# Kernel tuning notes

Hardware: AMD Instinct MI355X
Metric: run time of the kernel (lower is better)

## Reference

```python
import jax, jax.numpy as jnp
import numpy as np

EPS = 1e-3  # keras LayerNormalization default epsilon

def _ln(x, gamma, beta):
    m = jnp.mean(x, axis=-1, keepdims=True)
    v = jnp.var(x, axis=-1, keepdims=True)
    return gamma * (x - m) * jax.lax.rsqrt(v + EPS) + beta

def setup_inputs() -> dict:
    B, T, F, H = 256, 128, 4, 512  # T*F must equal H (skip-connection constraint in context GRN)
    D = T * F
    key = jax.random.key(0)
    ks = jax.random.split(key, 16)
    s = lambda fan: 1.0 / np.sqrt(fan)
    inp = {
        "inputs": jax.random.normal(ks[0], (B, T, F), jnp.float32),
        # context GRN (input dim D = T*F = H)
        "W1c": jax.random.normal(ks[1], (D, H), jnp.float32) * s(D),
        "b1c": jnp.zeros((H,), jnp.float32),
        "W2c": jax.random.normal(ks[2], (H, H), jnp.float32) * s(H),
        "b2c": jnp.zeros((H,), jnp.float32),
        "Wgc": jax.random.normal(ks[3], (H, H), jnp.float32) * s(H),
        "bgc": jnp.zeros((H,), jnp.float32),
        "gamma_c": jnp.ones((H,), jnp.float32),
        "beta_c": jnp.zeros((H,), jnp.float32),
        # softmax variable-selection head
        "Wsel": jax.random.normal(ks[4], (H, F), jnp.float32) * s(H),
        "bsel": jnp.zeros((F,), jnp.float32),
        # F per-variable GRNs, batched over leading F axis (input dim 1)
        "w1": jax.random.normal(ks[5], (F, H), jnp.float32),
        "b1": jnp.zeros((F, H), jnp.float32),
        "W2": jax.random.normal(ks[6], (F, H, H), jnp.float32) * s(H),
        "b2": jnp.zeros((F, H), jnp.float32),
        "Wg": jax.random.normal(ks[7], (F, H, H), jnp.float32) * s(H),
        "bg": jnp.zeros((F, H), jnp.float32),
        "gamma": jnp.ones((F, H), jnp.float32),
        "beta": jnp.zeros((F, H), jnp.float32),
    }
    return inp

def reference(inputs, W1c, b1c, W2c, b2c, Wgc, bgc, gamma_c, beta_c,
              Wsel, bsel, w1, b1, W2, b2, Wg, bg, gamma, beta):
    B, T, F = inputs.shape
    # ---- context GRN on flattened inputs (skip == flat since T*F == H) ----
    flat = inputs.reshape(B, T * F)
    x = jax.nn.elu(flat @ W1c + b1c)
    x = x @ W2c + b2c
    g = jax.nn.sigmoid(x @ Wgc + bgc)
    ctx = _ln(g * x + (1.0 - g) * flat, gamma_c, beta_c)
    # ---- softmax selection weights over variables ----
    sel = jax.nn.softmax(ctx @ Wsel + bsel)  # [B, F]
    # ---- per-variable GRNs, batched over F (input is scalar per variable) ----
    v = inputs[..., None]                              # [B,T,F,1] (skip path)
    x1 = jax.nn.elu(v * w1 + b1)                       # [B,T,F,H]
    x2 = jnp.einsum('btfh,fhk->btfk', x1, W2) + b2     # dense2
    gv = jax.nn.sigmoid(jnp.einsum('btfh,fhk->btfk', x2, Wg) + bg)
    gated = gv * x2 + (1.0 - gv) * v                   # skip broadcasts [B,T,F,1]
    tv = _ln(gated, gamma, beta)                       # [B,T,F,H]
    # ---- weighted sum over variables ----
    selected = jnp.einsum('btfh,bf->bth', tv, sel)     # [B,T,H]
    sel_weights = jnp.tile(sel[:, None, None, :], (1, T, 1, 1))  # [B,T,1,F]
    return selected, sel_weights
```

## Files before the change

### kernel.cpp

```cpp
#include <hip/hip_runtime.h>
#include <math.h>


#define H 512
#define NF 4
#define MTOT 32768

typedef unsigned short u16;
typedef unsigned int u32;
typedef __attribute__((ext_vector_type(8))) short short8;
typedef __attribute__((ext_vector_type(4))) float f32x4;
typedef __attribute__((ext_vector_type(4))) u32 u32x4;

__device__ __forceinline__ u16 f2bf(float x) {
  union { float f; u32 u; } v; v.f = x;
  return (u16)((v.u + 0x7fffu + ((v.u >> 16) & 1u)) >> 16);
}
__device__ __forceinline__ float bf2f(u32 h16) {
  union { u32 u; float f; } v; v.u = h16 << 16;
  return v.f;
}
__device__ __forceinline__ float elu_f(float x) {
  return x > 0.0f ? x : (__expf(x) - 1.0f);
}
__device__ __forceinline__ float sigmoid_f(float x) {
  return __builtin_amdgcn_rcpf(1.0f + __expf(-x));
}
__device__ __forceinline__ u32 cvtpk(float lo, float hi) {
  u32 r;
  asm("v_cvt_pk_bf16_f32 %0, %1, %2" : "=v"(r) : "v"(lo), "v"(hi));
  return r;
}
template <int CTRL>
__device__ __forceinline__ float dppadd(float v) {
  int t = __builtin_amdgcn_update_dpp(0, __float_as_int(v), CTRL, 0xF, 0xF, true);
  return v + __int_as_float(t);
}
__device__ __forceinline__ float red16(float v) {
  v = dppadd<0xB1>(v);
  v = dppadd<0x4E>(v);
  v = dppadd<0x141>(v);
  v = dppadd<0x140>(v);
  return v;
}

__device__ __forceinline__ void glld16(const void* g, void* l) {
  __builtin_amdgcn_global_load_lds(
      (const __attribute__((address_space(1))) u32*)(unsigned long long)(uintptr_t)g,
      (__attribute__((address_space(3))) u32*)(u32)(uintptr_t)l, 16, 0, 0);
}

#define MFMA16(a, b, c) __builtin_amdgcn_mfma_f32_16x16x32_bf16((a), (b), (c), 0, 0, 0)

__device__ __forceinline__ int sA_idx(int m, int n) {
  return m * 512 + ((((n >> 3) ^ (m & 7)) << 3) + (n & 7));
}

__device__ __forceinline__ void gridbar(u32* cnt, u32 target) {
  __syncthreads();
  __threadfence();
  if (threadIdx.x == 0) {
    __hip_atomic_fetch_add(cnt, 1u, __ATOMIC_RELEASE, __HIP_MEMORY_SCOPE_AGENT);
    while (__hip_atomic_load(cnt, __ATOMIC_ACQUIRE, __HIP_MEMORY_SCOPE_AGENT) < target)
      __builtin_amdgcn_s_sleep(8);
  }
  __syncthreads();
  __threadfence();
}

struct TileCtx {
  int tid, wid, lane, quad, col;
};

__global__ __launch_bounds__(256)
void pack_all(const float* __restrict__ W2, const float* __restrict__ Wg,
              const float* __restrict__ W1c, const float* __restrict__ W2c,
              const float* __restrict__ Wgc,
              u16* __restrict__ W2p, u16* __restrict__ Wgp, u16* __restrict__ Cp,
              u32* __restrict__ bar) {
  int g = blockIdx.x * 256 + threadIdx.x;
  if (g == 0) { bar[0] = 0; bar[1] = 0; }
  int r = g & 32767; int mat = g >> 15;
  if (mat >= 11) return;
  const float* src; u16* dst;
  if (mat < 4)      { src = W2 + (size_t)mat * 262144;       dst = W2p + (size_t)mat * 262144; }
  else if (mat < 8) { src = Wg + (size_t)(mat - 4) * 262144; dst = Wgp + (size_t)(mat - 4) * 262144; }
  else              { src = (mat == 8 ? W1c : (mat == 9 ? W2c : Wgc));
                      dst = Cp + (size_t)(mat - 8) * 262144; }
  dst += (size_t)r * 8;
  int lane = r & 63;
  int n, k0;
  if (mat == 8 || mat == 9) {
    int nb = r >> 12, kk = (r >> 8) & 15, ntg = (r >> 6) & 3;
    n  = nb * 64 + ntg * 16 + (lane & 15);
    k0 = kk * 32 + (lane >> 4) * 8;
  } else {
    int nt = (r >> 6) & 31, kk = (r >> 11) & 15;
    n  = nt * 16 + (lane & 15);
    k0 = kk * 32 + (lane >> 4) * 8;
  }
  short8 pk;
  #pragma unroll
  for (int j = 0; j < 8; ++j) pk[j] = (short)f2bf(src[(size_t)(k0 + j) * H + n]);
  *(short8*)dst = pk;
}

__device__ __forceinline__ void slab_kloop(const TileCtx& c, const u16* Wslab,
                                           u16* sA, u16* sB0, u16* sB1,
                                           f32x4 acc[4]) {
  #pragma unroll 1
  for (int kk = 0; kk < 16; ++kk) {
    if (kk < 15)
      glld16(Wslab + (kk + 1) * 2048 + c.tid * 8,
             (((kk + 1) & 1) ? sB1 : sB0) + c.tid * 8);
    const u16* bp = ((kk & 1) ? sB1 : sB0) + c.wid * 512 + c.lane * 8;
    short8 bb = *(const short8*)(bp);
    const int kq = kk * 4 + c.quad;
    const int s0 = (kq ^ (c.col & 7)) * 8;
    short8 a0 = *(const short8*)&sA[(     c.col) * 512 + s0];
    short8 a1 = *(const short8*)&sA[(16 + c.col) * 512 + s0];
    short8 a2 = *(const short8*)&sA[(32 + c.col) * 512 + s0];
    short8 a3 = *(const short8*)&sA[(48 + c.col) * 512 + s0];
    acc[0] = MFMA16(a0, bb, acc[0]);
    acc[1] = MFMA16(a1, bb, acc[1]);
    acc[2] = MFMA16(a2, bb, acc[2]);
    acc[3] = MFMA16(a3, bb, acc[3]);
    __syncthreads();
  }
}

__global__ __launch_bounds__(256)
void ctx_fused(const float* __restrict__ in, const u16* __restrict__ Cp,
               const float* __restrict__ b1c, const float* __restrict__ b2c,
               const float* __restrict__ bgc,
               const float* __restrict__ gamma_c, const float* __restrict__ beta_c,
               const float* __restrict__ Wsel, const float* __restrict__ bsel,
               u16* __restrict__ x1g, u16* __restrict__ xg,
               float* __restrict__ sel_ws, float* __restrict__ selw_out,
               u32* __restrict__ bar)
{
  __shared__ __align__(16) u16 smem[49152];
  TileCtx c;
  c.tid = threadIdx.x; c.wid = c.tid >> 6; c.lane = c.tid & 63;
  c.quad = c.lane >> 4; c.col = c.lane & 15;
  const int blk = blockIdx.x;
  const int mb = blk >> 3, nb = blk & 7;
  const int m0 = mb * 64;

  {
    u16* const sA  = smem;
    u16* const sB0 = smem + 32768;
    u16* const sB1 = smem + 34816;
    const u16* Wslab = Cp + (size_t)nb * 32768;
    glld16(Wslab + c.tid * 8, sB0 + c.tid * 8);
    {
      const int m = c.tid >> 2;
      const int kb = (c.tid & 3) * 128;
      const float* rowp = in + (size_t)(m0 + m) * H;
      #pragma unroll
      for (int gg = 0; gg < 16; ++gg) {
        const int ge = (gg + (c.tid & 3) * 4) & 15;
        const int k = kb + ge * 8;
        float4 v0 = *(const float4*)&rowp[k];
        float4 v1 = *(const float4*)&rowp[k + 4];
        u32x4 pk4;
        pk4.x = cvtpk(v0.x, v0.y); pk4.y = cvtpk(v0.z, v0.w);
        pk4.z = cvtpk(v1.x, v1.y); pk4.w = cvtpk(v1.z, v1.w);
        const int grp = (k >> 3) ^ (m & 7);
        *(u32x4*)&sA[m * 512 + grp * 8] = pk4;
      }
    }
    __syncthreads();
    f32x4 acc[4];
    #pragma unroll
    for (int mt = 0; mt < 4; ++mt) acc[mt] = (f32x4){0,0,0,0};
    slab_kloop(c, Wslab, sA, sB0, sB1, acc);
    const int n = nb * 64 + c.wid * 16 + c.col;
    const float bv = b1c[n];
    #pragma unroll
    for (int mt = 0; mt < 4; ++mt)
      #pragma unroll
      for (int reg = 0; reg < 4; ++reg) {
        const int m = m0 + mt * 16 + c.quad * 4 + reg;
        x1g[(size_t)m * H + n] = f2bf(elu_f(acc[mt][reg] + bv));
      }
  }
  gridbar(bar + 0, 32);

  {
    u16* const sA  = smem;
    u16* const sB0 = smem + 32768;
    u16* const sB1 = smem + 34816;
    const u16* Wslab = Cp + 262144 + (size_t)nb * 32768;
    glld16(Wslab + c.tid * 8, sB0 + c.tid * 8);
    {
      const int m = c.tid >> 2;
      const int kb = (c.tid & 3) * 128;
      const u16* rowp = x1g + (size_t)(m0 + m) * H;
      #pragma unroll
      for (int gg = 0; gg < 16; ++gg) {
        const int ge = (gg + (c.tid & 3) * 4) & 15;
        const int k = kb + ge * 8;
        short8 w = *(const short8*)&rowp[k];
        const int grp = (k >> 3) ^ (m & 7);
        *(short8*)&sA[m * 512 + grp * 8] = w;
      }
    }
    __syncthreads();
    f32x4 acc[4];
    #pragma unroll
    for (int mt = 0; mt < 4; ++mt) acc[mt] = (f32x4){0,0,0,0};
    slab_kloop(c, Wslab, sA, sB0, sB1, acc);
    const int n = nb * 64 + c.wid * 16 + c.col;
    const float bv = b2c[n];
    #pragma unroll
    for (int mt = 0; mt < 4; ++mt)
      #pragma unroll
      for (int reg = 0; reg < 4; ++reg) {
        const int m = m0 + mt * 16 + c.quad * 4 + reg;
        xg[(size_t)m * H + n] = f2bf(acc[mt][reg] + bv);
      }
  }
  gridbar(bar + 1, 32);
  if (blk >= 16) return;

  {
    u16* const sA  = smem;
    u16* const sB0 = smem + 8192;
    u16* const sB1 = smem + 24576;
    float* const sRedF = (float*)sB0;
    float* const sZp  = sRedF + 1024;
    float* const sZf  = sRedF + 1792;
    float* const sSel = sRedF + 1952;
    const int b0 = blk * 16;
    const u16* Wgcp = Cp + 524288;

    #pragma unroll
    for (int i = 0; i < 8; ++i)
      glld16(Wgcp + (i * 256 + c.tid) * 8, sB0 + (i * 256 + c.tid) * 8);

    {
      const int m  = c.tid >> 4;
      const int kb = (c.tid & 15) * 32;
      const u16* rowp = xg + (size_t)(b0 + m) * H;
      #pragma unroll
      for (int gg = 0; gg < 4; ++gg) {
        const int ge = (gg + (c.tid & 15)) & 3;
        const int k = kb + ge * 8;
        short8 w = *(const short8*)&rowp[k];
        const int grp = (k >> 3) ^ (m & 7);
        *(short8*)&sA[m * 512 + grp * 8] = w;
      }
    }
    __syncthreads();

    f32x4 acc8[8];
    #pragma unroll
    for (int j = 0; j < 8; ++j) acc8[j] = (f32x4){0,0,0,0};

    #pragma unroll 1
    for (int kk = 0; kk < 16; ++kk) {
      if (kk < 15) {
        const u16* src = Wgcp + (kk + 1) * 16384;
        u16* dst = ((kk + 1) & 1) ? sB1 : sB0;
        #pragma unroll
        for (int i = 0; i < 8; ++i)
          glld16(src + (i * 256 + c.tid) * 8, dst + (i * 256 + c.tid) * 8);
      }
      const u16* bp = (kk & 1) ? sB1 : sB0;
      short8 bb[8];
      #pragma unroll
      for (int j = 0; j < 8; ++j)
        bb[j] = *(const short8*)(bp + ((c.wid * 8 + j) * 64 + c.lane) * 8);
      const int kq = kk * 4 + c.quad;
      const int s0 = (kq ^ (c.col & 7)) * 8;
      short8 a0 = *(const short8*)&sA[c.col * 512 + s0];
      #pragma unroll
      for (int j = 0; j < 8; ++j) acc8[j] = MFMA16(a0, bb[j], acc8[j]);
      __syncthreads();
    }

    {
      float bv[8];
      #pragma unroll
      for (int j = 0; j < 8; ++j) bv[j] = bgc[c.wid * 128 + j * 16 + c.col];
      #pragma unroll
      for (int j = 0; j < 8; ++j) {
        const int n = c.wid * 128 + j * 16 + c.col;
        #pragma unroll
        for (int reg = 0; reg < 4; ++reg) {
          const int m = c.quad * 4 + reg;
          const float xv = bf2f(sA[sA_idx(m, n)]);
          const float fl = in[(size_t)(b0 + m) * H + n];
          const float gv = sigmoid_f(acc8[j][reg] + bv[j]);
          acc8[j][reg] = gv * xv + (1.0f - gv) * fl;
        }
      }
    }

    {
      float rs[4], rq[4];
      #pragma unroll
      for (int reg = 0; reg < 4; ++reg) {
        rs[reg] = 0.f; rq[reg] = 0.f;
        #pragma unroll
        for (int j = 0; j < 8; ++j) {
          const float gt = acc8[j][reg];
          rs[reg] += gt; rq[reg] += gt * gt;
        }
        rs[reg] = red16(rs[reg]);
        rq[reg] = red16(rq[reg]);
      }
      if (c.col == 0) {
        #pragma unroll
        for (int reg = 0; reg < 4; ++reg) {
          const int m = c.quad * 4 + reg;
          float2 sq; sq.x = rs[reg]; sq.y = rq[reg];
          *(float2*)&sRedF[m * 20 + c.wid * 2] = sq;
        }
      }
    }
    __syncthreads();
    if (c.tid < 16) {
      const int row = c.tid;
      float s = 0.f, q = 0.f;
      #pragma unroll
      for (int jj = 0; jj < 2; ++jj) {
        float4 v = *(float4*)&sRedF[row * 20 + jj * 4];
        s += v.x + v.z; q += v.y + v.w;
      }
      const float mu = s * (1.0f / H);
      const float rstd = rsqrtf(q * (1.0f / H) - mu * mu + 1e-3f);
      float2 mr; mr.x = mu; mr.y = rstd;
      *(float2*)&sRedF[640 + row * 2] = mr;
    }
    __syncthreads();

    {
      float gm[8], bt[8]; float4 ws4[8];
      #pragma unroll
      for (int j = 0; j < 8; ++j) {
        const int n = c.wid * 128 + j * 16 + c.col;
        gm[j] = gamma_c[n]; bt[j] = beta_c[n];
        ws4[j] = *(const float4*)&Wsel[n * NF];
      }
      #pragma unroll
      for (int reg = 0; reg < 4; ++reg) {
        const int m = c.quad * 4 + reg;
        float2 mr = *(float2*)&sRedF[640 + m * 2];
        float zp[4] = {0.f, 0.f, 0.f, 0.f};
        #pragma unroll
        for (int j = 0; j < 8; ++j) {
          const float ctxv = gm[j] * ((acc8[j][reg] - mr.x) * mr.y) + bt[j];
          zp[0] = fmaf(ctxv, ws4[j].x, zp[0]);
          zp[1] = fmaf(ctxv, ws4[j].y, zp[1]);
          zp[2] = fmaf(ctxv, ws4[j].z, zp[2]);
          zp[3] = fmaf(ctxv, ws4[j].w, zp[3]);
        }
        #pragma unroll
        for (int f = 0; f < 4; ++f) zp[f] = red16(zp[f]);
        if (c.col == 0) {
          #pragma unroll
          for (int f = 0; f < 4; ++f) sZp[(m * 4 + c.wid) * 4 + f] = zp[f];
        }
      }
    }
    __syncthreads();
    if (c.tid < 64) {
      const int m = c.tid >> 2, f = c.tid & 3;
      float z = bsel[f];
      #pragma unroll
      for (int w = 0; w < 4; ++w) z += sZp[(m * 4 + w) * 4 + f];
      sZf[m * 4 + f] = z;
    }
    __syncthreads();
    if (c.tid < 16) {
      const int m = c.tid;
      float z0 = sZf[m*4], z1 = sZf[m*4+1], z2 = sZf[m*4+2], z3 = sZf[m*4+3];
      float mx = fmaxf(fmaxf(z0, z1), fmaxf(z2, z3));
      float e0 = __expf(z0-mx), e1 = __expf(z1-mx), e2 = __expf(z2-mx), e3 = __expf(z3-mx);
      float inv = __builtin_amdgcn_rcpf(e0 + e1 + e2 + e3);
      sSel[m*4]   = e0*inv; sSel[m*4+1] = e1*inv;
      sSel[m*4+2] = e2*inv; sSel[m*4+3] = e3*inv;
      sel_ws[(b0+m)*NF]   = e0*inv; sel_ws[(b0+m)*NF+1] = e1*inv;
      sel_ws[(b0+m)*NF+2] = e2*inv; sel_ws[(b0+m)*NF+3] = e3*inv;
    }
    __syncthreads();
    {
      const int m = c.tid >> 4;
      const int jb = (c.tid & 15) * 32;
      float4 v; v.x = sSel[m*4]; v.y = sSel[m*4+1]; v.z = sSel[m*4+2]; v.w = sSel[m*4+3];
      #pragma unroll
      for (int j = 0; j < 8; ++j)
        *(float4*)&selw_out[(size_t)(b0 + m) * H + jb + j * 4] = v;
    }
  }
}


__device__ __forceinline__ void stage_slice(int wid, int lane, const u16* chunk, u16* dstbuf) {
  const u16* src = chunk + wid * 2048 + lane * 8;
  u16* dst = dstbuf + lane * 8;
  glld16(src,        dst);
  glld16(src + 512,  dst + 512);
  glld16(src + 1024, dst + 1024);
  glld16(src + 1536, dst + 1536);
}

__device__ __forceinline__ void gemm_kloop_nb(const TileCtx& c, const u16* Wp,
                                              const u16* sA, u16* sBw,
                                              f32x4 acc[4][4]) {
  #pragma unroll 1
  for (int kk = 0; kk < 16; ++kk) {
    if (kk < 15) {
      stage_slice(c.wid, c.lane, Wp + (kk + 1) * 16384, sBw + ((kk + 1) & 1) * 2048);
      asm volatile("s_waitcnt vmcnt(4)" ::: "memory");
    } else {
      asm volatile("s_waitcnt vmcnt(0)" ::: "memory");
    }
    __builtin_amdgcn_sched_barrier(0);
    const u16* bp = sBw + (kk & 1) * 2048 + c.lane * 8;
    short8 bb[4];
    #pragma unroll
    for (int nt = 0; nt < 4; ++nt) bb[nt] = *(const short8*)(bp + nt * 512);
    const int kq = kk * 4 + c.quad;
    const int s0 = (kq ^ (c.col & 7)) * 8;
    __builtin_amdgcn_s_setprio(1);
    #pragma unroll
    for (int mt = 0; mt < 4; ++mt) {
      short8 a = *(const short8*)&sA[(mt * 16 + c.col) * 512 + s0];
      #pragma unroll
      for (int nt = 0; nt < 4; ++nt)
        acc[mt][nt] = MFMA16(a, bb[nt], acc[mt][nt]);
    }
    __builtin_amdgcn_s_setprio(0);
  }
}

__device__ __forceinline__ void store_x2_pair_n(const TileCtx& c, u16* sA,
                                                int mt, int n, u32 o01, u32 o23) {
  const bool even = (c.lane & 1) == 0;
  const u32 send = even ? o23 : o01;
  const u32 recv = (u32)__builtin_amdgcn_update_dpp(0, (int)send, 0xB1, 0xF, 0xF, true);
  const u32 hi = even ? recv : o23;
  const u32 lo = even ? o01 : recv;
  const u32 dlo = __builtin_amdgcn_perm(hi, lo, 0x05040100u);
  const u32 dhi = __builtin_amdgcn_perm(hi, lo, 0x07060302u);
  const int np = n & ~1;
  const int mA = mt * 16 + c.quad * 4 + (even ? 0 : 2);
  const int iA = mA * 512 + ((((np >> 3) ^ (mA & 7)) << 3) + (np & 7));
  const int mB = mA + 1;
  const int iB = mB * 512 + ((((np >> 3) ^ (mB & 7)) << 3) + (np & 7));
  *(u32*)&sA[iA] = dlo;
  *(u32*)&sA[iB] = dhi;
}

__device__ __forceinline__ void ln_reduce8(const TileCtx& c, float* sRedF,
                                           f32x4 acc[4][4]) {
  #pragma unroll
  for (int mt = 0; mt < 4; ++mt) {
    float rs[4], rq[4];
    #pragma unroll
    for (int reg = 0; reg < 4; ++reg) {
      rs[reg] = 0.f; rq[reg] = 0.f;
      #pragma unroll
      for (int nt = 0; nt < 4; ++nt) {
        const float gt = acc[mt][nt][reg];
        rs[reg] += gt; rq[reg] += gt * gt;
      }
      rs[reg] = red16(rs[reg]);
      rq[reg] = red16(rq[reg]);
    }
    if (c.col == 0) {
      #pragma unroll
      for (int reg = 0; reg < 4; ++reg) {
        const int m = mt * 16 + c.quad * 4 + reg;
        float2 sq; sq.x = rs[reg]; sq.y = rq[reg];
        *(float2*)&sRedF[m * 20 + c.wid * 2] = sq;
      }
    }
  }
  __syncthreads();
  if (c.tid < 64) {
    const int row = c.tid;
    float s = 0.f, q = 0.f;
    #pragma unroll
    for (int jj = 0; jj < 4; ++jj) {
      float4 v = *(float4*)&sRedF[row * 20 + jj * 4];
      s += v.x + v.z; q += v.y + v.w;
    }
    const float mu = s * (1.0f / H);
    const float rstd = rsqrtf(q * (1.0f / H) - mu * mu + 1e-3f);
    float2 mr; mr.x = mu; mr.y = rstd;
    *(float2*)&sRedF[1280 + row * 2] = mr;
  }
  __syncthreads();
}

__global__ __launch_bounds__(512, 2)
void vsn_mfma(const float* __restrict__ in,
              const float* __restrict__ w1, const float* __restrict__ b1,
              const float* __restrict__ b2, const float* __restrict__ bg,
              const float* __restrict__ gamma, const float* __restrict__ beta,
              const u16* __restrict__ W2p, const u16* __restrict__ Wgp,
              const float* __restrict__ sel_ws,
              float* __restrict__ out)
{
  __shared__ __align__(16) u16 smem[65536];
  u16* const sA  = smem;
  u16* const sB  = smem + 32768;
  float* const sRedF = (float*)smem;

  TileCtx c;
  c.tid = threadIdx.x; c.wid = c.tid >> 6; c.lane = c.tid & 63;
  c.quad = c.lane >> 4; c.col = c.lane & 15;
  u16* const sBw = sB + c.wid * 4096;
  const int row0 = blockIdx.x * 64;
  const int bidx = row0 >> 7;

  f32x4 outacc[4][4];
  #pragma unroll
  for (int mt = 0; mt < 4; ++mt)
    #pragma unroll
    for (int nt = 0; nt < 4; ++nt) outacc[mt][nt] = (f32x4){0,0,0,0};

  stage_slice(c.wid, c.lane, W2p, sBw);

  #pragma unroll 1
  for (int f = 0; f < NF; ++f) {
    const u16* W2f = W2p + (size_t)f * 262144;
    const u16* Wgf = Wgp + (size_t)f * 262144;

    {
      const int m  = c.tid >> 3;
      const int kb = (c.tid & 7) * 64;
      const float v = in[(size_t)(row0 + m) * NF + f];
      const float* w1f = w1 + f * H;
      const float* b1f = b1 + f * H;
      #pragma unroll
      for (int gg = 0; gg < 8; ++gg) {
        const int ge = (gg + (c.tid & 7)) & 7;
        const int k = kb + ge * 8;
        float4 wv0 = *(const float4*)&w1f[k];
        float4 wv1 = *(const float4*)&w1f[k + 4];
        float4 bv0 = *(const float4*)&b1f[k];
        float4 bv1 = *(const float4*)&b1f[k + 4];
        u32x4 pk4;
        pk4.x = cvtpk(elu_f(fmaf(v, wv0.x, bv0.x)), elu_f(fmaf(v, wv0.y, bv0.y)));
        pk4.y = cvtpk(elu_f(fmaf(v, wv0.z, bv0.z)), elu_f(fmaf(v, wv0.w, bv0.w)));
        pk4.z = cvtpk(elu_f(fmaf(v, wv1.x, bv1.x)), elu_f(fmaf(v, wv1.y, bv1.y)));
        pk4.w = cvtpk(elu_f(fmaf(v, wv1.z, bv1.z)), elu_f(fmaf(v, wv1.w, bv1.w)));
        const int grp = (k >> 3) ^ (m & 7);
        *(u32x4*)&sA[m * 512 + grp * 8] = pk4;
      }
    }
    __syncthreads();

    f32x4 acc[4][4];
    #pragma unroll
    for (int mt = 0; mt < 4; ++mt)
      #pragma unroll
      for (int nt = 0; nt < 4; ++nt) acc[mt][nt] = (f32x4){0,0,0,0};

    gemm_kloop_nb(c, W2f, sA, sBw, acc);
    __syncthreads();

    stage_slice(c.wid, c.lane, Wgf, sBw);

    u32 x2p[4][4][2];
    {
      float bv[4];
      #pragma unroll
      for (int nt = 0; nt < 4; ++nt) bv[nt] = b2[f * H + c.wid * 64 + nt * 16 + c.col];
      #pragma unroll
      for (int mt = 0; mt < 4; ++mt)
        #pragma unroll
        for (int nt = 0; nt < 4; ++nt) {
          const u32 o01 = cvtpk(acc[mt][nt][0] + bv[nt], acc[mt][nt][1] + bv[nt]);
          const u32 o23 = cvtpk(acc[mt][nt][2] + bv[nt], acc[mt][nt][3] + bv[nt]);
          x2p[mt][nt][0] = o01; x2p[mt][nt][1] = o23;
          store_x2_pair_n(c, sA, mt, c.wid * 64 + nt * 16 + c.col, o01, o23);
        }
    }
    __syncthreads();

    #pragma unroll
    for (int mt = 0; mt < 4; ++mt)
      #pragma unroll
      for (int nt = 0; nt < 4; ++nt) acc[mt][nt] = (f32x4){0,0,0,0};
    gemm_kloop_nb(c, Wgf, sA, sBw, acc);

    {
      const float selw = sel_ws[bidx * NF + f];
      float bv[4];
      #pragma unroll
      for (int nt = 0; nt < 4; ++nt) bv[nt] = bg[f * H + c.wid * 64 + nt * 16 + c.col];
      #pragma unroll
      for (int mt = 0; mt < 4; ++mt) {
        float vr[4];
        #pragma unroll
        for (int reg = 0; reg < 4; ++reg)
          vr[reg] = in[(size_t)(row0 + mt * 16 + c.quad * 4 + reg) * NF + f];
        #pragma unroll
        for (int nt = 0; nt < 4; ++nt)
          #pragma unroll
          for (int reg = 0; reg < 4; ++reg) {
            const u32 w = x2p[mt][nt][reg >> 1];
            const float x2v = bf2f((reg & 1) ? (w >> 16) : (w & 0xffffu));
            const float gv = sigmoid_f(acc[mt][nt][reg] + bv[nt]);
            acc[mt][nt][reg] = gv * x2v + (1.0f - gv) * vr[reg];
          }
      }
      __syncthreads();
      ln_reduce8(c, sRedF, acc);
      float gm[4], bt[4];
      #pragma unroll
      for (int nt = 0; nt < 4; ++nt) {
        const int n = f * H + c.wid * 64 + nt * 16 + c.col;
        gm[nt] = gamma[n]; bt[nt] = beta[n];
      }
      #pragma unroll
      for (int mt = 0; mt < 4; ++mt)
        #pragma unroll
        for (int reg = 0; reg < 4; ++reg) {
          const int m = mt * 16 + c.quad * 4 + reg;
          float2 mr = *(float2*)&sRedF[1280 + m * 2];
          #pragma unroll
          for (int nt = 0; nt < 4; ++nt) {
            const float tv = gm[nt] * ((acc[mt][nt][reg] - mr.x) * mr.y) + bt[nt];
            outacc[mt][nt][reg] = fmaf(selw, tv, outacc[mt][nt][reg]);
          }
        }
      if (f < NF - 1)
        stage_slice(c.wid, c.lane, W2p + (size_t)(f + 1) * 262144, sBw);
      __syncthreads();
    }
  }

  #pragma unroll
  for (int mt = 0; mt < 4; ++mt)
    #pragma unroll
    for (int reg = 0; reg < 4; ++reg) {
      const int m = row0 + mt * 16 + c.quad * 4 + reg;
      #pragma unroll
      for (int nt = 0; nt < 4; ++nt)
        out[(size_t)m * H + c.wid * 64 + nt * 16 + c.col] = outacc[mt][nt][reg];
    }
}

extern "C" void kernel_launch(void* const* d_in, const int* in_sizes, int n_in,
                              void* d_out, int out_size, void* d_ws, size_t ws_size,
                              hipStream_t stream) {
  const float* in_     = (const float*)d_in[0];
  const float* W1c     = (const float*)d_in[1];
  const float* b1c     = (const float*)d_in[2];
  const float* W2c     = (const float*)d_in[3];
  const float* b2c     = (const float*)d_in[4];
  const float* Wgc     = (const float*)d_in[5];
  const float* bgc     = (const float*)d_in[6];
  const float* gamma_c = (const float*)d_in[7];
  const float* beta_c  = (const float*)d_in[8];
  const float* Wsel    = (const float*)d_in[9];
  const float* bsel    = (const float*)d_in[10];
  const float* w1      = (const float*)d_in[11];
  const float* b1v     = (const float*)d_in[12];
  const float* W2      = (const float*)d_in[13];
  const float* b2v     = (const float*)d_in[14];
  const float* Wg      = (const float*)d_in[15];
  const float* bgv     = (const float*)d_in[16];
  const float* gma     = (const float*)d_in[17];
  const float* bta     = (const float*)d_in[18];

  float* out_sel = (float*)d_out;
  float* out_w   = (float*)d_out + (size_t)MTOT * H;

  float* sel_ws = (float*)d_ws;
  u16*   W2p    = (u16*)((char*)d_ws + 4096);
  u16*   Wgp    = W2p + (size_t)NF * H * H;
  u16*   Cp     = Wgp + (size_t)NF * H * H;
  u16*   x1g    = Cp + 3 * 262144;
  u16*   xg     = x1g + 131072;
  u32*   bar    = (u32*)(xg + 131072);

  hipLaunchKernelGGL(pack_all, dim3(1408), dim3(256), 0, stream,
                     W2, Wg, W1c, W2c, Wgc, W2p, Wgp, Cp, bar);
  hipLaunchKernelGGL(ctx_fused, dim3(32), dim3(256), 0, stream,
                     in_, Cp, b1c, b2c, bgc, gamma_c, beta_c, Wsel, bsel,
                     x1g, xg, sel_ws, out_w, bar);
  hipLaunchKernelGGL(vsn_mfma, dim3(MTOT / 64), dim3(512), 0, stream,
                     in_, w1, b1v, b2v, bgv, gma, bta, W2p, Wgp, sel_ws, out_sel);
}
```

Before: 359.3 us.

## Fold context GRN into main kernel as per-block GEMVs, drop grid-barrier kernel

Removes the separate 32-block context kernel, along with its grid-wide barriers and global intermediates. Each block of the main VSN kernel now recomputes the context GRN, layer norm and softmax selection for its batch row. This is done as three bf16 GEMVs over the packed weights, with the selection weights kept in shared memory. The goal is to remove a poorly occupied serial kernel and a launch, at the cost of redundant context computation per block (about 1.5 MB of weight reads each) that sits on the critical path before the main GEMMs.

```diff
diff --git a/kernel.cpp b/kernel.cpp
--- a/kernel.cpp
+++ b/kernel.cpp
@@ -52,22 +52,6 @@
 
 #define MFMA16(a, b, c) __builtin_amdgcn_mfma_f32_16x16x32_bf16((a), (b), (c), 0, 0, 0)
 
-__device__ __forceinline__ int sA_idx(int m, int n) {
-  return m * 512 + ((((n >> 3) ^ (m & 7)) << 3) + (n & 7));
-}
-
-__device__ __forceinline__ void gridbar(u32* cnt, u32 target) {
-  __syncthreads();
-  __threadfence();
-  if (threadIdx.x == 0) {
-    __hip_atomic_fetch_add(cnt, 1u, __ATOMIC_RELEASE, __HIP_MEMORY_SCOPE_AGENT);
-    while (__hip_atomic_load(cnt, __ATOMIC_ACQUIRE, __HIP_MEMORY_SCOPE_AGENT) < target)
-      __builtin_amdgcn_s_sleep(8);
-  }
-  __syncthreads();
-  __threadfence();
-}
-
 struct TileCtx {
   int tid, wid, lane, quad, col;
 };
@@ -76,10 +60,8 @@
 void pack_all(const float* __restrict__ W2, const float* __restrict__ Wg,
               const float* __restrict__ W1c, const float* __restrict__ W2c,
               const float* __restrict__ Wgc,
-              u16* __restrict__ W2p, u16* __restrict__ Wgp, u16* __restrict__ Cp,
-              u32* __restrict__ bar) {
+              u16* __restrict__ W2p, u16* __restrict__ Wgp, u16* __restrict__ Cp) {
   int g = blockIdx.x * 256 + threadIdx.x;
-  if (g == 0) { bar[0] = 0; bar[1] = 0; }
   int r = g & 32767; int mat = g >> 15;
   if (mat >= 11) return;
   const float* src; u16* dst;
@@ -105,296 +87,47 @@
   *(short8*)dst = pk;
 }
 
-__device__ __forceinline__ void slab_kloop(const TileCtx& c, const u16* Wslab,
-                                           u16* sA, u16* sB0, u16* sB1,
-                                           f32x4 acc[4]) {
-  #pragma unroll 1
-  for (int kk = 0; kk < 16; ++kk) {
-    if (kk < 15)
-      glld16(Wslab + (kk + 1) * 2048 + c.tid * 8,
-             (((kk + 1) & 1) ? sB1 : sB0) + c.tid * 8);
-    const u16* bp = ((kk & 1) ? sB1 : sB0) + c.wid * 512 + c.lane * 8;
-    short8 bb = *(const short8*)(bp);
-    const int kq = kk * 4 + c.quad;
-    const int s0 = (kq ^ (c.col & 7)) * 8;
-    short8 a0 = *(const short8*)&sA[(     c.col) * 512 + s0];
-    short8 a1 = *(const short8*)&sA[(16 + c.col) * 512 + s0];
-    short8 a2 = *(const short8*)&sA[(32 + c.col) * 512 + s0];
-    short8 a3 = *(const short8*)&sA[(48 + c.col) * 512 + s0];
-    acc[0] = MFMA16(a0, bb, acc[0]);
-    acc[1] = MFMA16(a1, bb, acc[1]);
-    acc[2] = MFMA16(a2, bb, acc[2]);
-    acc[3] = MFMA16(a3, bb, acc[3]);
-    __syncthreads();
-  }
-}
-
-__global__ __launch_bounds__(256)
-void ctx_fused(const float* __restrict__ in, const u16* __restrict__ Cp,
-               const float* __restrict__ b1c, const float* __restrict__ b2c,
-               const float* __restrict__ bgc,
-               const float* __restrict__ gamma_c, const float* __restrict__ beta_c,
-               const float* __restrict__ Wsel, const float* __restrict__ bsel,
-               u16* __restrict__ x1g, u16* __restrict__ xg,
-               float* __restrict__ sel_ws, float* __restrict__ selw_out,
-               u32* __restrict__ bar)
-{
-  __shared__ __align__(16) u16 smem[49152];
-  TileCtx c;
-  c.tid = threadIdx.x; c.wid = c.tid >> 6; c.lane = c.tid & 63;
-  c.quad = c.lane >> 4; c.col = c.lane & 15;
-  const int blk = blockIdx.x;
-  const int mb = blk >> 3, nb = blk & 7;
-  const int m0 = mb * 64;
-
-  {
-    u16* const sA  = smem;
-    u16* const sB0 = smem + 32768;
-    u16* const sB1 = smem + 34816;
-    const u16* Wslab = Cp + (size_t)nb * 32768;
-    glld16(Wslab + c.tid * 8, sB0 + c.tid * 8);
-    {
-      const int m = c.tid >> 2;
-      const int kb = (c.tid & 3) * 128;
-      const float* rowp = in + (size_t)(m0 + m) * H;
-      #pragma unroll
-      for (int gg = 0; gg < 16; ++gg) {
-        const int ge = (gg + (c.tid & 3) * 4) & 15;
-        const int k = kb + ge * 8;
-        float4 v0 = *(const float4*)&rowp[k];
-        float4 v1 = *(const float4*)&rowp[k + 4];
-        u32x4 pk4;
-        pk4.x = cvtpk(v0.x, v0.y); pk4.y = cvtpk(v0.z, v0.w);
-        pk4.z = cvtpk(v1.x, v1.y); pk4.w = cvtpk(v1.z, v1.w);
-        const int grp = (k >> 3) ^ (m & 7);
-        *(u32x4*)&sA[m * 512 + grp * 8] = pk4;
-      }
-    }
-    __syncthreads();
-    f32x4 acc[4];
-    #pragma unroll
-    for (int mt = 0; mt < 4; ++mt) acc[mt] = (f32x4){0,0,0,0};
-    slab_kloop(c, Wslab, sA, sB0, sB1, acc);
-    const int n = nb * 64 + c.wid * 16 + c.col;
-    const float bv = b1c[n];
-    #pragma unroll
-    for (int mt = 0; mt < 4; ++mt)
-      #pragma unroll
-      for (int reg = 0; reg < 4; ++reg) {
-        const int m = m0 + mt * 16 + c.quad * 4 + reg;
-        x1g[(size_t)m * H + n] = f2bf(elu_f(acc[mt][reg] + bv));
-      }
-  }
-  gridbar(bar + 0, 32);
-
-  {
-    u16* const sA  = smem;
-    u16* const sB0 = smem + 32768;
-    u16* const sB1 = smem + 34816;
-    const u16* Wslab = Cp + 262144 + (size_t)nb * 32768;
-    glld16(Wslab + c.tid * 8, sB0 + c.tid * 8);
-    {
-      const int m = c.tid >> 2;
-      const int kb = (c.tid & 3) * 128;
-      const u16* rowp = x1g + (size_t)(m0 + m) * H;
-      #pragma unroll
-      for (int gg = 0; gg < 16; ++gg) {
-        const int ge = (gg + (c.tid & 3) * 4) & 15;
-        const int k = kb + ge * 8;
-        short8 w = *(const short8*)&rowp[k];
-        const int grp = (k >> 3) ^ (m & 7);
-        *(short8*)&sA[m * 512 + grp * 8] = w;
-      }
-    }
-    __syncthreads();
-    f32x4 acc[4];
-    #pragma unroll
-    for (int mt = 0; mt < 4; ++mt) acc[mt] = (f32x4){0,0,0,0};
-    slab_kloop(c, Wslab, sA, sB0, sB1, acc);
-    const int n = nb * 64 + c.wid * 16 + c.col;
-    const float bv = b2c[n];
-    #pragma unroll
-    for (int mt = 0; mt < 4; ++mt)
-      #pragma unroll
-      for (int reg = 0; reg < 4; ++reg) {
-        const int m = m0 + mt * 16 + c.quad * 4 + reg;
-        xg[(size_t)m * H + n] = f2bf(acc[mt][reg] + bv);
-      }
-  }
-  gridbar(bar + 1, 32);
-  if (blk >= 16) return;
-
-  {
-    u16* const sA  = smem;
-    u16* const sB0 = smem + 8192;
-    u16* const sB1 = smem + 24576;
-    float* const sRedF = (float*)sB0;
-    float* const sZp  = sRedF + 1024;
-    float* const sZf  = sRedF + 1792;
-    float* const sSel = sRedF + 1952;
-    const int b0 = blk * 16;
-    const u16* Wgcp = Cp + 524288;
-
-    #pragma unroll
-    for (int i = 0; i < 8; ++i)
-      glld16(Wgcp + (i * 256 + c.tid) * 8, sB0 + (i * 256 + c.tid) * 8);
-
-    {
-      const int m  = c.tid >> 4;
-      const int kb = (c.tid & 15) * 32;
-      const u16* rowp = xg + (size_t)(b0 + m) * H;
-      #pragma unroll
-      for (int gg = 0; gg < 4; ++gg) {
-        const int ge = (gg + (c.tid & 15)) & 3;
-        const int k = kb + ge * 8;
-        short8 w = *(const short8*)&rowp[k];
-        const int grp = (k >> 3) ^ (m & 7);
-        *(short8*)&sA[m * 512 + grp * 8] = w;
-      }
-    }
-    __syncthreads();
-
-    f32x4 acc8[8];
-    #pragma unroll
-    for (int j = 0; j < 8; ++j) acc8[j] = (f32x4){0,0,0,0};
-
-    #pragma unroll 1
-    for (int kk = 0; kk < 16; ++kk) {
-      if (kk < 15) {
-        const u16* src = Wgcp + (kk + 1) * 16384;
-        u16* dst = ((kk + 1) & 1) ? sB1 : sB0;
-        #pragma unroll
-        for (int i = 0; i < 8; ++i)
-          glld16(src + (i * 256 + c.tid) * 8, dst + (i * 256 + c.tid) * 8);
-      }
-      const u16* bp = (kk & 1) ? sB1 : sB0;
-      short8 bb[8];
-      #pragma unroll
-      for (int j = 0; j < 8; ++j)
-        bb[j] = *(const short8*)(bp + ((c.wid * 8 + j) * 64 + c.lane) * 8);
-      const int kq = kk * 4 + c.quad;
-      const int s0 = (kq ^ (c.col & 7)) * 8;
-      short8 a0 = *(const short8*)&sA[c.col * 512 + s0];
-      #pragma unroll
-      for (int j = 0; j < 8; ++j) acc8[j] = MFMA16(a0, bb[j], acc8[j]);
-      __syncthreads();
-    }
-
-    {
-      float bv[8];
-      #pragma unroll
-      for (int j = 0; j < 8; ++j) bv[j] = bgc[c.wid * 128 + j * 16 + c.col];
-      #pragma unroll
-      for (int j = 0; j < 8; ++j) {
-        const int n = c.wid * 128 + j * 16 + c.col;
-        #pragma unroll
-        for (int reg = 0; reg < 4; ++reg) {
-          const int m = c.quad * 4 + reg;
-          const float xv = bf2f(sA[sA_idx(m, n)]);
-          const float fl = in[(size_t)(b0 + m) * H + n];
-          const float gv = sigmoid_f(acc8[j][reg] + bv[j]);
-          acc8[j][reg] = gv * xv + (1.0f - gv) * fl;
-        }
-      }
-    }
-
-    {
-      float rs[4], rq[4];
-      #pragma unroll
-      for (int reg = 0; reg < 4; ++reg) {
-        rs[reg] = 0.f; rq[reg] = 0.f;
-        #pragma unroll
-        for (int j = 0; j < 8; ++j) {
-          const float gt = acc8[j][reg];
-          rs[reg] += gt; rq[reg] += gt * gt;
-        }
-        rs[reg] = red16(rs[reg]);
-        rq[reg] = red16(rq[reg]);
-      }
-      if (c.col == 0) {
-        #pragma unroll
-        for (int reg = 0; reg < 4; ++reg) {
-          const int m = c.quad * 4 + reg;
-          float2 sq; sq.x = rs[reg]; sq.y = rq[reg];
-          *(float2*)&sRedF[m * 20 + c.wid * 2] = sq;
-        }
-      }
-    }
-    __syncthreads();
-    if (c.tid < 16) {
-      const int row = c.tid;
-      float s = 0.f, q = 0.f;
-      #pragma unroll
-      for (int jj = 0; jj < 2; ++jj) {
-        float4 v = *(float4*)&sRedF[row * 20 + jj * 4];
-        s += v.x + v.z; q += v.y + v.w;
-      }
-      const float mu = s * (1.0f / H);
-      const float rstd = rsqrtf(q * (1.0f / H) - mu * mu + 1e-3f);
-      float2 mr; mr.x = mu; mr.y = rstd;
-      *(float2*)&sRedF[640 + row * 2] = mr;
-    }
-    __syncthreads();
-
-    {
-      float gm[8], bt[8]; float4 ws4[8];
-      #pragma unroll
-      for (int j = 0; j < 8; ++j) {
-        const int n = c.wid * 128 + j * 16 + c.col;
-        gm[j] = gamma_c[n]; bt[j] = beta_c[n];
-        ws4[j] = *(const float4*)&Wsel[n * NF];
-      }
-      #pragma unroll
-      for (int reg = 0; reg < 4; ++reg) {
-        const int m = c.quad * 4 + reg;
-        float2 mr = *(float2*)&sRedF[640 + m * 2];
-        float zp[4] = {0.f, 0.f, 0.f, 0.f};
-        #pragma unroll
-        for (int j = 0; j < 8; ++j) {
-          const float ctxv = gm[j] * ((acc8[j][reg] - mr.x) * mr.y) + bt[j];
-          zp[0] = fmaf(ctxv, ws4[j].x, zp[0]);
-          zp[1] = fmaf(ctxv, ws4[j].y, zp[1]);
-          zp[2] = fmaf(ctxv, ws4[j].z, zp[2]);
-          zp[3] = fmaf(ctxv, ws4[j].w, zp[3]);
-        }
-        #pragma unroll
-        for (int f = 0; f < 4; ++f) zp[f] = red16(zp[f]);
-        if (c.col == 0) {
-          #pragma unroll
-          for (int f = 0; f < 4; ++f) sZp[(m * 4 + c.wid) * 4 + f] = zp[f];
-        }
-      }
-    }
-    __syncthreads();
-    if (c.tid < 64) {
-      const int m = c.tid >> 2, f = c.tid & 3;
-      float z = bsel[f];
-      #pragma unroll
-      for (int w = 0; w < 4; ++w) z += sZp[(m * 4 + w) * 4 + f];
-      sZf[m * 4 + f] = z;
-    }
-    __syncthreads();
-    if (c.tid < 16) {
-      const int m = c.tid;
-      float z0 = sZf[m*4], z1 = sZf[m*4+1], z2 = sZf[m*4+2], z3 = sZf[m*4+3];
-      float mx = fmaxf(fmaxf(z0, z1), fmaxf(z2, z3));
-      float e0 = __expf(z0-mx), e1 = __expf(z1-mx), e2 = __expf(z2-mx), e3 = __expf(z3-mx);
-      float inv = __builtin_amdgcn_rcpf(e0 + e1 + e2 + e3);
-      sSel[m*4]   = e0*inv; sSel[m*4+1] = e1*inv;
-      sSel[m*4+2] = e2*inv; sSel[m*4+3] = e3*inv;
-      sel_ws[(b0+m)*NF]   = e0*inv; sel_ws[(b0+m)*NF+1] = e1*inv;
-      sel_ws[(b0+m)*NF+2] = e2*inv; sel_ws[(b0+m)*NF+3] = e3*inv;
-    }
-    __syncthreads();
-    {
-      const int m = c.tid >> 4;
-      const int jb = (c.tid & 15) * 32;
-      float4 v; v.x = sSel[m*4]; v.y = sSel[m*4+1]; v.z = sSel[m*4+2]; v.w = sSel[m*4+3];
-      #pragma unroll
-      for (int j = 0; j < 8; ++j)
-        *(float4*)&selw_out[(size_t)(b0 + m) * H + jb + j * 4] = v;
-    }
-  }
+
+__device__ __forceinline__ float gemv512_slab(const u16* __restrict__ W,
+                                              const float* __restrict__ vec, int n) {
+  const u16* base = W + (size_t)(n >> 6) * 32768 + ((n >> 4) & 3) * 512 + (n & 15) * 8;
+  float acc = 0.f;
+  #pragma unroll 4
+  for (int kg = 0; kg < 64; ++kg) {
+    short8 w = *(const short8*)(base + (kg >> 2) * 2048 + (kg & 3) * 128);
+    float4 v0 = *(const float4*)&vec[kg * 8];
+    float4 v1 = *(const float4*)&vec[kg * 8 + 4];
+    acc = fmaf(v0.x, bf2f((u16)w[0]), acc);
+    acc = fmaf(v0.y, bf2f((u16)w[1]), acc);
+    acc = fmaf(v0.z, bf2f((u16)w[2]), acc);
+    acc = fmaf(v0.w, bf2f((u16)w[3]), acc);
+    acc = fmaf(v1.x, bf2f((u16)w[4]), acc);
+    acc = fmaf(v1.y, bf2f((u16)w[5]), acc);
+    acc = fmaf(v1.z, bf2f((u16)w[6]), acc);
+    acc = fmaf(v1.w, bf2f((u16)w[7]), acc);
+  }
+  return acc;
+}
+
+__device__ __forceinline__ float gemv512_chunk(const u16* __restrict__ W,
+                                               const float* __restrict__ vec, int n) {
+  const u16* base = W + (size_t)(n >> 4) * 512 + (n & 15) * 8;
+  float acc = 0.f;
+  #pragma unroll 4
+  for (int kg = 0; kg < 64; ++kg) {
+    short8 w = *(const short8*)(base + (kg >> 2) * 16384 + (kg & 3) * 128);
+    float4 v0 = *(const float4*)&vec[kg * 8];
+    float4 v1 = *(const float4*)&vec[kg * 8 + 4];
+    acc = fmaf(v0.x, bf2f((u16)w[0]), acc);
+    acc = fmaf(v0.y, bf2f((u16)w[1]), acc);
+    acc = fmaf(v0.z, bf2f((u16)w[2]), acc);
+    acc = fmaf(v0.w, bf2f((u16)w[3]), acc);
+    acc = fmaf(v1.x, bf2f((u16)w[4]), acc);
+    acc = fmaf(v1.y, bf2f((u16)w[5]), acc);
+    acc = fmaf(v1.z, bf2f((u16)w[6]), acc);
+    acc = fmaf(v1.w, bf2f((u16)w[7]), acc);
+  }
+  return acc;
 }
 
 
@@ -503,13 +236,19 @@
               const float* __restrict__ b2, const float* __restrict__ bg,
               const float* __restrict__ gamma, const float* __restrict__ beta,
               const u16* __restrict__ W2p, const u16* __restrict__ Wgp,
-              const float* __restrict__ sel_ws,
-              float* __restrict__ out)
+              const u16* __restrict__ Cp,
+              const float* __restrict__ b1c, const float* __restrict__ b2c,
+              const float* __restrict__ bgc,
+              const float* __restrict__ gamma_c, const float* __restrict__ beta_c,
+              const float* __restrict__ Wsel, const float* __restrict__ bsel,
+              float* __restrict__ out,
+              float* __restrict__ selw_out)
 {
-  __shared__ __align__(16) u16 smem[65536];
+  __shared__ __align__(16) u16 smem[65552];
   u16* const sA  = smem;
   u16* const sB  = smem + 32768;
   float* const sRedF = (float*)smem;
+  float* const sSelP = (float*)&smem[65536];
 
   TileCtx c;
   c.tid = threadIdx.x; c.wid = c.tid >> 6; c.lane = c.tid & 63;
@@ -517,6 +256,69 @@
   u16* const sBw = sB + c.wid * 4096;
   const int row0 = blockIdx.x * 64;
   const int bidx = row0 >> 7;
+
+  {
+    float* const sF  = (float*)(smem + 32768);
+    float* const sV1 = sF + 512;
+    float* const sV2 = sV1 + 512;
+    float* const sP  = sV2 + 512;
+    const int n = c.tid;
+    const float flat_n = in[(size_t)bidx * 512 + n];
+    sF[n] = flat_n;
+    __syncthreads();
+    const float x1 = elu_f(gemv512_slab(Cp, sF, n) + b1c[n]);
+    sV1[n] = x1;
+    __syncthreads();
+    const float xv = gemv512_slab(Cp + 262144, sV1, n) + b2c[n];
+    sV2[n] = xv;
+    __syncthreads();
+    const float gp = gemv512_chunk(Cp + 524288, sV2, n) + bgc[n];
+    const float gv = sigmoid_f(gp);
+    const float gated = gv * xv + (1.0f - gv) * flat_n;
+    {
+      float s = red16(gated), q = red16(gated * gated);
+      if ((c.lane & 15) == 0) { sP[c.tid >> 4] = s; sP[32 + (c.tid >> 4)] = q; }
+    }
+    __syncthreads();
+    if (c.tid == 0) {
+      float ss = 0.f, qq = 0.f;
+      #pragma unroll
+      for (int i = 0; i < 32; ++i) { ss += sP[i]; qq += sP[32 + i]; }
+      const float mu = ss * (1.0f / H);
+      const float rstd = rsqrtf(qq * (1.0f / H) - mu * mu + 1e-3f);
+      sP[64] = mu; sP[65] = rstd;
+    }
+    __syncthreads();
+    const float ctxv = gamma_c[n] * ((gated - sP[64]) * sP[65]) + beta_c[n];
+    {
+      float4 ws = *(const float4*)&Wsel[n * NF];
+      float z0 = red16(ctxv * ws.x), z1 = red16(ctxv * ws.y);
+      float z2 = red16(ctxv * ws.z), z3 = red16(ctxv * ws.w);
+      if ((c.lane & 15) == 0) {
+        float4 zz; zz.x = z0; zz.y = z1; zz.z = z2; zz.w = z3;
+        *(float4*)&sP[68 + (c.tid >> 4) * 4] = zz;
+      }
+    }
+    __syncthreads();
+    if (c.tid == 0) {
+      float z0 = bsel[0], z1 = bsel[1], z2 = bsel[2], z3 = bsel[3];
+      #pragma unroll
+      for (int i = 0; i < 32; ++i) {
+        float4 zz = *(float4*)&sP[68 + i * 4];
+        z0 += zz.x; z1 += zz.y; z2 += zz.z; z3 += zz.w;
+      }
+      const float mx = fmaxf(fmaxf(z0, z1), fmaxf(z2, z3));
+      const float e0 = __expf(z0-mx), e1 = __expf(z1-mx);
+      const float e2 = __expf(z2-mx), e3 = __expf(z3-mx);
+      const float inv = __builtin_amdgcn_rcpf(e0 + e1 + e2 + e3);
+      sSelP[0] = e0*inv; sSelP[1] = e1*inv; sSelP[2] = e2*inv; sSelP[3] = e3*inv;
+    }
+    __syncthreads();
+    if (c.tid < 64) {
+      float4 v; v.x = sSelP[0]; v.y = sSelP[1]; v.z = sSelP[2]; v.w = sSelP[3];
+      *(float4*)&selw_out[(size_t)(row0 + c.tid) * NF] = v;
+    }
+  }
 
   f32x4 outacc[4][4];
   #pragma unroll
@@ -591,7 +393,7 @@
     gemm_kloop_nb(c, Wgf, sA, sBw, acc);
 
     {
-      const float selw = sel_ws[bidx * NF + f];
+      const float selw = sSelP[f];
       float bv[4];
       #pragma unroll
       for (int nt = 0; nt < 4; ++nt) bv[nt] = bg[f * H + c.wid * 64 + nt * 16 + c.col];
@@ -674,19 +476,14 @@
   float* out_sel = (float*)d_out;
   float* out_w   = (float*)d_out + (size_t)MTOT * H;
 
-  float* sel_ws = (float*)d_ws;
-  u16*   W2p    = (u16*)((char*)d_ws + 4096);
+  u16*   W2p    = (u16*)d_ws;
   u16*   Wgp    = W2p + (size_t)NF * H * H;
   u16*   Cp     = Wgp + (size_t)NF * H * H;
-  u16*   x1g    = Cp + 3 * 262144;
-  u16*   xg     = x1g + 131072;
-  u32*   bar    = (u32*)(xg + 131072);
 
   hipLaunchKernelGGL(pack_all, dim3(1408), dim3(256), 0, stream,
-                     W2, Wg, W1c, W2c, Wgc, W2p, Wgp, Cp, bar);
-  hipLaunchKernelGGL(ctx_fused, dim3(32), dim3(256), 0, stream,
-                     in_, Cp, b1c, b2c, bgc, gamma_c, beta_c, Wsel, bsel,
-                     x1g, xg, sel_ws, out_w, bar);
+                     W2, Wg, W1c, W2c, Wgc, W2p, Wgp, Cp);
   hipLaunchKernelGGL(vsn_mfma, dim3(MTOT / 64), dim3(512), 0, stream,
-                     in_, w1, b1v, b2v, bgv, gma, bta, W2p, Wgp, sel_ws, out_sel);
-}
+                     in_, w1, b1v, b2v, bgv, gma, bta, W2p, Wgp,
+                     Cp, b1c, b2c, bgc, gamma_c, beta_c, Wsel, bsel,
+                     out_sel, out_w);
+}
```

Result: no change. 364.8 us (+1.5%).
